# Kernel tuning notes

Measured on AMD Instinct MI355X. Metric: run time of the kernel, lower is better.

The kernel has to match this reference:

```python
import jax, jax.numpy as jnp
import numpy as np

B, S, N, F = 8, 512, 1024, 32   # batch, seq_len, num_nodes, num_features
H = 64                          # hidden_dim
G0 = H // 2                     # first gcn output (32)
K = 3                           # tcn kernel size


def setup_inputs() -> dict:
    key = jax.random.key(0)
    ks = jax.random.split(key, 20)

    def w(k, shape, fan_in):
        return (jax.random.normal(k, shape, dtype=jnp.float32)
                * jnp.asarray(1.0 / np.sqrt(fan_in), jnp.float32))

    return {
        "x":   jax.random.normal(ks[0], (B, S, N, F), dtype=jnp.float32),
        "adj": jax.random.uniform(ks[1], (N, N), dtype=jnp.float32),
        # GCN layer 0: F -> G0 ; layer 1: G0 -> H  (weights stored [in,out])
        "gcn_w0": w(ks[2], (F, G0), F),  "gcn_b0": jnp.zeros((G0,), jnp.float32),
        "gcn_w1": w(ks[3], (G0, H), G0), "gcn_b1": jnp.zeros((H,), jnp.float32),
        # TCN conv weights [out_ch, in_ch, k]
        "conv_w0": w(ks[4], (H, H, K), H * K), "conv_b0": jnp.zeros((H,), jnp.float32),
        "conv_w1": w(ks[5], (H, H, K), H * K), "conv_b1": jnp.zeros((H,), jnp.float32),
        "conv_w2": w(ks[6], (H, H, K), H * K), "conv_b2": jnp.zeros((H,), jnp.float32),
        # fusion Linear(H->H), predictor Linear(H->H//2) -> Linear(H//2->1)
        "fusion_w": w(ks[7], (H, H), H),       "fusion_b": jnp.zeros((H,), jnp.float32),
        "pred_w1": w(ks[8], (H, H // 2), H),   "pred_b1": jnp.zeros((H // 2,), jnp.float32),
        "pred_w2": w(ks[9], (H // 2, 1), H // 2), "pred_b2": jnp.zeros((1,), jnp.float32),
    }


def _normalize_adj(adj):
    # A' = A + I ; D^{-1/2} A' D^{-1/2}   (inf -> 0 guard as in torch code)
    a = adj + jnp.eye(adj.shape[0], dtype=adj.dtype)
    deg = a.sum(axis=1)
    dis = jnp.where(deg > 0, jax.lax.rsqrt(deg), jnp.zeros_like(deg))
    return dis[:, None] * a * dis[None, :]


def _causal_conv(x, w, b, dilation):
    # x: [B, C_in, S], w: [C_out, C_in, K] -> left-pad only == torch pad+trim
    pad = (w.shape[-1] - 1) * dilation
    y = jax.lax.conv_general_dilated(
        x, w, window_strides=(1,), padding=[(pad, 0)],
        rhs_dilation=(dilation,), dimension_numbers=("NCH", "OIH", "NCH"))
    return jax.nn.relu(y + b[None, :, None])  # dropout = identity (eval)


def reference(x, adj, gcn_w0, gcn_b0, gcn_w1, gcn_b1,
              conv_w0, conv_b0, conv_w1, conv_b1, conv_w2, conv_b2,
              fusion_w, fusion_b, pred_w1, pred_b1, pred_w2, pred_b2):
    # adjacency normalization is identical for every timestep/layer: do once
    an = _normalize_adj(adj)  # [N, N]

    # GCN over all timesteps at once (vectorized over the seq loop)
    h = jax.nn.relu(jnp.einsum("mn,bsnf->bsmf", an, x @ gcn_w0) + gcn_b0)
    h = jax.nn.relu(jnp.einsum("mn,bsnf->bsmf", an, h @ gcn_w1) + gcn_b1)

    spatial = h.mean(axis=2)                    # [B, S, H] mean over nodes
    t = jnp.transpose(spatial, (0, 2, 1))       # [B, H, S]

    t = _causal_conv(t, conv_w0, conv_b0, dilation=1)
    t = _causal_conv(t, conv_w1, conv_b1, dilation=2)
    t = _causal_conv(t, conv_w2, conv_b2, dilation=4)

    last = t[:, :, -1]                          # [B, H]
    fused = jax.nn.relu(last @ fusion_w + fusion_b)
    out = jax.nn.relu(fused @ pred_w1 + pred_b1) @ pred_w2 + pred_b2
    return out                                  # [B, 1]
```

## Files before the change

### kernel.cpp

```cpp
#include <hip/hip_runtime.h>
#include <hip/hip_bf16.h>

#define B_   8
#define S_   512
#define N_   1024
#define F_   32
#define H_   64
#define G0_  32
#define T_   15
#define BT_  (B_ * T_)
#define C1_  (BT_ * G0_)

typedef __bf16 bfx8 __attribute__((ext_vector_type(8)));
typedef __bf16 bfx4 __attribute__((ext_vector_type(4)));
typedef float  f32x4 __attribute__((ext_vector_type(4)));

__device__ __forceinline__ void async16(void* l, const void* g) {
    __builtin_amdgcn_global_load_lds(
        (__attribute__((address_space(1))) const void*)g,
        (__attribute__((address_space(3))) void*)l, 16, 0, 0);
}

__global__ void k_deg(const float* __restrict__ adj, float* __restrict__ dis) {
    int r = blockIdx.x;
    int tid = threadIdx.x;
    const float* row = adj + (size_t)r * N_;
    float p = 0.f;
    for (int n = tid; n < N_; n += 256) p += row[n];
    __shared__ float red[256];
    red[tid] = p;
    __syncthreads();
    for (int s = 128; s > 0; s >>= 1) {
        if (tid < s) red[tid] += red[tid + s];
        __syncthreads();
    }
    if (tid == 0) {
        float deg = red[0] + 1.0f;
        dis[r] = (deg > 0.f) ? rsqrtf(deg) : 0.f;
    }
}

__global__ void k_an(const float* __restrict__ adj, const float* __restrict__ dis,
                     __bf16* __restrict__ an) {
    int idx = (blockIdx.x * 256 + threadIdx.x) * 4;
    int m = idx >> 10, n0 = idx & 1023;
    float dm = dis[m];
    float4 a = *(const float4*)&adj[idx];
    float v[4] = {a.x, a.y, a.z, a.w};
    bfx4 o;
#pragma unroll
    for (int j = 0; j < 4; ++j) {
        float vv = v[j] + ((n0 + j) == m ? 1.0f : 0.0f);
        o[j] = (__bf16)(dm * vv * dis[n0 + j]);
    }
    *(bfx4*)&an[idx] = o;
}

__global__ void k_xw0(const float* __restrict__ x, const float* __restrict__ w0,
                      __bf16* __restrict__ xw0t) {
    int bt = blockIdx.y, n0 = blockIdx.x * 32, tid = threadIdx.x;
    int b = bt / T_, tau = bt % T_, s = S_ - T_ + tau;
    __shared__ float xs[32][33];
    __shared__ float w0s[32 * 32];
    const float* xp = x + ((size_t)((b * S_ + s) * N_ + n0)) * F_;
    {
        int r = tid >> 3, c4 = (tid & 7) * 4;
        *(float4*)&xs[r][c4] = *(const float4*)&xp[r * 32 + c4];
        *(float4*)&w0s[tid * 4] = *(const float4*)&w0[tid * 4];
    }
    __syncthreads();
    int g = tid >> 3, nb = (tid & 7) * 4;
    float a0 = 0.f, a1 = 0.f, a2 = 0.f, a3 = 0.f;
#pragma unroll
    for (int f = 0; f < 32; ++f) {
        float wv = w0s[f * 32 + g];
        a0 += xs[nb + 0][f] * wv;
        a1 += xs[nb + 1][f] * wv;
        a2 += xs[nb + 2][f] * wv;
        a3 += xs[nb + 3][f] * wv;
    }
    bfx4 o;
    o[0] = (__bf16)a0; o[1] = (__bf16)a1; o[2] = (__bf16)a2; o[3] = (__bf16)a3;
    *(bfx4*)&xw0t[(size_t)(bt * 32 + g) * N_ + n0 + nb] = o;
}

template <int MODE>
__global__ __launch_bounds__(256) void k_mm(const __bf16* __restrict__ A,
                                            const __bf16* __restrict__ Bm,
                                            void* __restrict__ Cv,
                                            const float* __restrict__ bias) {
    __shared__ __bf16 As[2][128 * 64];
    __shared__ __bf16 Bs[2][128 * 64];
    int tid = threadIdx.x;
    int lane = tid & 63, wv = tid >> 6;
    int rb = blockIdx.y * 128;
    int cb = blockIdx.x * 128;
    int wr = (wv >> 1) * 64, wc = (wv & 1) * 64;

    f32x4 acc[4][4] = {};

    int srow = lane >> 3;
    int scol = ((lane & 7) ^ (srow & 7)) * 8;
    const __bf16* gA = A  + (size_t)(rb + wv * 32 + srow) * 1024 + scol;
    const __bf16* gB = Bm + (size_t)(cb + wv * 32 + srow) * 1024 + scol;

    const int c16 = lane & 15;
    const int qa  = (lane >> 4) * 8;

#pragma unroll
    for (int i = 0; i < 4; ++i) {
        async16(&As[0][(wv * 32 + i * 8) * 64], gA + (size_t)i * 8 * 1024);
        async16(&Bs[0][(wv * 32 + i * 8) * 64], gB + (size_t)i * 8 * 1024);
    }
    __syncthreads();

    int cur = 0;
    for (int t = 0; t < 16; ++t) {
        if (t + 1 < 16) {
            const __bf16* pA = gA + (t + 1) * 64;
            const __bf16* pB = gB + (t + 1) * 64;
#pragma unroll
            for (int i = 0; i < 4; ++i) {
                async16(&As[cur ^ 1][(wv * 32 + i * 8) * 64], pA + (size_t)i * 8 * 1024);
                async16(&Bs[cur ^ 1][(wv * 32 + i * 8) * 64], pB + (size_t)i * 8 * 1024);
            }
        }
#pragma unroll
        for (int kk = 0; kk < 2; ++kk) {
            bfx8 af[4], bfv[4];
#pragma unroll
            for (int r = 0; r < 4; ++r) {
                int row = wr + 16 * r + c16;
                int col = (kk * 64 + qa * 2) ^ ((row & 7) << 4);
                af[r] = *(const bfx8*)((const char*)&As[cur][0] + row * 128 + col);
            }
#pragma unroll
            for (int c = 0; c < 4; ++c) {
                int row = wc + 16 * c + c16;
                int col = (kk * 64 + qa * 2) ^ ((row & 7) << 4);
                bfv[c] = *(const bfx8*)((const char*)&Bs[cur][0] + row * 128 + col);
            }
#pragma unroll
            for (int r = 0; r < 4; ++r)
#pragma unroll
                for (int c = 0; c < 4; ++c)
                    acc[r][c] = __builtin_amdgcn_mfma_f32_16x16x32_bf16(
                        af[r], bfv[c], acc[r][c], 0, 0, 0);
        }
        __syncthreads();
        cur ^= 1;
    }

    int quad = lane >> 4;
    if (MODE == 1) {
        __bf16* C = (__bf16*)Cv;
        float be = bias[c16], bo = bias[c16 + 16];
#pragma unroll
        for (int cj = 0; cj < 4; ++cj) {
            size_t cc = (size_t)(cb + wc + 16 * cj + c16);
            float bg = (cj & 1) ? bo : be;
#pragma unroll
            for (int r = 0; r < 4; ++r) {
                int m4 = rb + wr + 16 * r + quad * 4;
                f32x4 v = acc[r][cj];
                bfx4 o;
#pragma unroll
                for (int j = 0; j < 4; ++j) o[j] = (__bf16)fmaxf(v[j] + bg, 0.f);
                *(bfx4*)&C[cc * 1024 + m4] = o;
            }
        }
    } else {
        float* C = (float*)Cv;
#pragma unroll
        for (int cj = 0; cj < 4; ++cj) {
            size_t cc = (size_t)(cb + wc + 16 * cj + c16);
#pragma unroll
            for (int r = 0; r < 4; ++r) {
                int m4 = rb + wr + 16 * r + quad * 4;
                *(f32x4*)&C[cc * 1024 + m4] = acc[r][cj];
            }
        }
    }
}

__global__ __launch_bounds__(256) void k_h2mean(const float* __restrict__ AGT,
                                                const float* __restrict__ w1,
                                                const float* __restrict__ b1,
                                                float* __restrict__ spatialP) {
    int blk = blockIdx.x;
    int bt = blk >> 2, q = blk & 3;
    int tid = threadIdx.x;
    int h = tid & 63, sub = tid >> 6;
    float w1r[32];
#pragma unroll
    for (int g = 0; g < 32; ++g) w1r[g] = w1[g * 64 + h];
    float bh = b1[h];
    float acc = 0.f;
    const float* base = AGT + (size_t)(bt * 32) * 1024 + q * 256 + sub * 64;
    for (int mq = 0; mq < 16; ++mq) {
        float v0 = bh, v1 = bh, v2 = bh, v3 = bh;
#pragma unroll
        for (int g = 0; g < 32; ++g) {
            float4 a = *(const float4*)(base + (size_t)g * 1024 + mq * 4);
            v0 += a.x * w1r[g];
            v1 += a.y * w1r[g];
            v2 += a.z * w1r[g];
            v3 += a.w * w1r[g];
        }
        acc += fmaxf(v0, 0.f) + fmaxf(v1, 0.f) + fmaxf(v2, 0.f) + fmaxf(v3, 0.f);
    }
    __shared__ float red[4][64];
    red[sub][h] = acc;
    __syncthreads();
    if (tid < 64) {
        spatialP[(size_t)blk * 64 + tid] =
            red[0][tid] + red[1][tid] + red[2][tid] + red[3][tid];
    }
}

__global__ __launch_bounds__(256) void k_head(const float* __restrict__ spatialP,
                       const float* __restrict__ cw0, const float* __restrict__ cb0,
                       const float* __restrict__ cw1, const float* __restrict__ cb1,
                       const float* __restrict__ cw2, const float* __restrict__ cb2,
                       const float* __restrict__ fw,  const float* __restrict__ fb,
                       const float* __restrict__ pw1, const float* __restrict__ pb1,
                       const float* __restrict__ pw2, const float* __restrict__ pb2,
                       float* __restrict__ out) {
    int b = blockIdx.x, tid = threadIdx.x;
    int o = tid & 63, ti = tid >> 6;
    __shared__ float wbuf[3 * 64 * 65];
    __shared__ float sp[15][64], c0s[15][64], c1s[15][64];
    __shared__ float lastv[64], fusedv[64], p1s[32];

    for (int j = tid; j < 15 * 64; j += 256) {
        int t = j >> 6, i = j & 63;
        const float* P = spatialP + ((size_t)(b * 15 + t) * 4) * 64 + i;
        ((float*)sp)[j] = (P[0] + P[64] + P[128] + P[192]) * (1.0f / N_);
    }
    for (int j = tid; j < 12288; j += 256) {
        int oo = j / 192, r = j % 192, ii = r / 3, kk = r % 3;
        wbuf[kk * 4160 + ii * 65 + oo] = cw0[j];
    }
    __syncthreads();
    for (int t4 = ti; t4 < 7; t4 += 4) {
        int t = 2 + 2 * t4;
        float v = cb0[o];
#pragma unroll
        for (int k = 0; k < 3; ++k) {
            const float* in = sp[t - 2 + k];
            const float* wk = &wbuf[k * 4160];
#pragma unroll
            for (int i = 0; i < 64; ++i) v += wk[i * 65 + o] * in[i];
        }
        c0s[t][o] = fmaxf(v, 0.f);
    }
    __syncthreads();
    for (int j = tid; j < 12288; j += 256) {
        int oo = j / 192, r = j % 192, ii = r / 3, kk = r % 3;
        wbuf[kk * 4160 + ii * 65 + oo] = cw1[j];
    }
    __syncthreads();
    if (ti < 3) {
        int t = 6 + 4 * ti;
        float v = cb1[o];
#pragma unroll
        for (int k = 0; k < 3; ++k) {
            const float* in = c0s[t - (2 - k) * 2];
            const float* wk = &wbuf[k * 4160];
#pragma unroll
            for (int i = 0; i < 64; ++i) v += wk[i * 65 + o] * in[i];
        }
        c1s[t][o] = fmaxf(v, 0.f);
    }
    __syncthreads();
    for (int j = tid; j < 12288; j += 256) {
        int oo = j / 192, r = j % 192, ii = r / 3, kk = r % 3;
        wbuf[kk * 4160 + ii * 65 + oo] = cw2[j];
    }
    __syncthreads();
    if (ti == 0) {
        float v = cb2[o];
#pragma unroll
        for (int k = 0; k < 3; ++k) {
            const float* in = c1s[14 - (2 - k) * 4];
            const float* wk = &wbuf[k * 4160];
#pragma unroll
            for (int i = 0; i < 64; ++i) v += wk[i * 65 + o] * in[i];
        }
        lastv[o] = fmaxf(v, 0.f);
    }
    __syncthreads();
    if (ti == 0) {
        float v = fb[o];
#pragma unroll
        for (int i = 0; i < 64; ++i) v += lastv[i] * fw[i * 64 + o];
        fusedv[o] = fmaxf(v, 0.f);
    }
    __syncthreads();
    if (tid < 32) {
        float v = pb1[tid];
#pragma unroll
        for (int i = 0; i < 64; ++i) v += fusedv[i] * pw1[i * 32 + tid];
        p1s[tid] = fmaxf(v, 0.f);
    }
    __syncthreads();
    if (tid == 0) {
        float v = pb2[0];
#pragma unroll
        for (int i = 0; i < 32; ++i) v += p1s[i] * pw2[i];
        out[b] = v;
    }
}

extern "C" void kernel_launch(void* const* d_in, const int* in_sizes, int n_in,
                              void* d_out, int out_size, void* d_ws, size_t ws_size,
                              hipStream_t stream) {
    (void)in_sizes; (void)n_in; (void)out_size; (void)ws_size;
    const float* x   = (const float*)d_in[0];
    const float* adj = (const float*)d_in[1];
    const float* w0  = (const float*)d_in[2];
    const float* b0  = (const float*)d_in[3];
    const float* w1  = (const float*)d_in[4];
    const float* b1  = (const float*)d_in[5];
    const float* cw0 = (const float*)d_in[6];
    const float* cb0 = (const float*)d_in[7];
    const float* cw1 = (const float*)d_in[8];
    const float* cb1 = (const float*)d_in[9];
    const float* cw2 = (const float*)d_in[10];
    const float* cb2 = (const float*)d_in[11];
    const float* fw  = (const float*)d_in[12];
    const float* fb  = (const float*)d_in[13];
    const float* pw1 = (const float*)d_in[14];
    const float* pb1 = (const float*)d_in[15];
    const float* pw2 = (const float*)d_in[16];
    const float* pb2 = (const float*)d_in[17];
    float* outp = (float*)d_out;

    char* w = (char*)d_ws;
    float*  dis      = (float*)(w);
    __bf16* an       = (__bf16*)(w + 4096);
    __bf16* xw0t     = (__bf16*)(w + 4096 + 2097152);
    __bf16* h1t      = (__bf16*)(w + 4096 + 2097152 + 7864320);
    float*  agt      = (float*) (w + 4096 + 2097152 + 2 * 7864320);
    float*  spatialP = (float*) (w + 4096 + 2097152 + 2 * 7864320 + 15728640);

    k_deg<<<N_, 256, 0, stream>>>(adj, dis);
    k_an<<<(N_ * N_) / 1024, 256, 0, stream>>>(adj, dis, an);
    k_xw0<<<dim3(N_ / 32, BT_), 256, 0, stream>>>(x, w0, xw0t);
    k_mm<1><<<dim3(C1_ / 128, N_ / 128), 256, 0, stream>>>(an, xw0t, (void*)h1t, b0);
    k_mm<0><<<dim3(C1_ / 128, N_ / 128), 256, 0, stream>>>(an, h1t, (void*)agt, nullptr);
    k_h2mean<<<BT_ * 4, 256, 0, stream>>>(agt, w1, b1, spatialP);
    k_head<<<B_, 256, 0, stream>>>(spatialP, cw0, cb0, cw1, cb1, cw2, cb2,
                                   fw, fb, pw1, pb1, pw2, pb2, outp);
}
```

Baseline: 712.5 us.

## Use eight-wave GEMM blocks and pre-transpose TCN conv weights in a prep kernel

```diff
diff --git a/kernel.cpp b/kernel.cpp
--- a/kernel.cpp
+++ b/kernel.cpp
@@ -54,6 +54,16 @@
         o[j] = (__bf16)(dm * vv * dis[n0 + j]);
     }
     *(bfx4*)&an[idx] = o;
+}
+
+__global__ void k_wprep(const float* __restrict__ cw0, const float* __restrict__ cw1,
+                        const float* __restrict__ cw2, float* __restrict__ wp) {
+    int idx = blockIdx.x * 256 + threadIdx.x;
+    if (idx >= 3 * 12480) return;
+    int layer = idx / 12480, r = idx % 12480;
+    int kk = r / 4160, r2 = r % 4160, ii = r2 / 65, oo = r2 % 65;
+    const float* src = (layer == 0) ? cw0 : ((layer == 1) ? cw1 : cw2);
+    wp[idx] = (oo < 64) ? src[oo * 192 + ii * 3 + kk] : 0.f;
 }
 
 __global__ void k_xw0(const float* __restrict__ x, const float* __restrict__ w0,
@@ -85,7 +95,7 @@
 }
 
 template <int MODE>
-__global__ __launch_bounds__(256) void k_mm(const __bf16* __restrict__ A,
+__global__ __launch_bounds__(512) void k_mm(const __bf16* __restrict__ A,
                                             const __bf16* __restrict__ Bm,
                                             void* __restrict__ Cv,
                                             const float* __restrict__ bias) {
@@ -95,22 +105,23 @@
     int lane = tid & 63, wv = tid >> 6;
     int rb = blockIdx.y * 128;
     int cb = blockIdx.x * 128;
-    int wr = (wv >> 1) * 64, wc = (wv & 1) * 64;
-
-    f32x4 acc[4][4] = {};
+    int wr = (wv >> 2) * 64;
+    int wc = (wv & 3) * 32;
+
+    f32x4 acc[4][2] = {};
 
     int srow = lane >> 3;
     int scol = ((lane & 7) ^ (srow & 7)) * 8;
-    const __bf16* gA = A  + (size_t)(rb + wv * 32 + srow) * 1024 + scol;
-    const __bf16* gB = Bm + (size_t)(cb + wv * 32 + srow) * 1024 + scol;
+    const __bf16* gA = A  + (size_t)(rb + wv * 16 + srow) * 1024 + scol;
+    const __bf16* gB = Bm + (size_t)(cb + wv * 16 + srow) * 1024 + scol;
 
     const int c16 = lane & 15;
     const int qa  = (lane >> 4) * 8;
 
 #pragma unroll
-    for (int i = 0; i < 4; ++i) {
-        async16(&As[0][(wv * 32 + i * 8) * 64], gA + (size_t)i * 8 * 1024);
-        async16(&Bs[0][(wv * 32 + i * 8) * 64], gB + (size_t)i * 8 * 1024);
+    for (int i = 0; i < 2; ++i) {
+        async16(&As[0][(wv * 16 + i * 8) * 64], gA + (size_t)i * 8 * 1024);
+        async16(&Bs[0][(wv * 16 + i * 8) * 64], gB + (size_t)i * 8 * 1024);
     }
     __syncthreads();
 
@@ -120,14 +131,14 @@
             const __bf16* pA = gA + (t + 1) * 64;
             const __bf16* pB = gB + (t + 1) * 64;
 #pragma unroll
-            for (int i = 0; i < 4; ++i) {
-                async16(&As[cur ^ 1][(wv * 32 + i * 8) * 64], pA + (size_t)i * 8 * 1024);
-                async16(&Bs[cur ^ 1][(wv * 32 + i * 8) * 64], pB + (size_t)i * 8 * 1024);
+            for (int i = 0; i < 2; ++i) {
+                async16(&As[cur ^ 1][(wv * 16 + i * 8) * 64], pA + (size_t)i * 8 * 1024);
+                async16(&Bs[cur ^ 1][(wv * 16 + i * 8) * 64], pB + (size_t)i * 8 * 1024);
             }
         }
 #pragma unroll
         for (int kk = 0; kk < 2; ++kk) {
-            bfx8 af[4], bfv[4];
+            bfx8 af[4], bfv[2];
 #pragma unroll
             for (int r = 0; r < 4; ++r) {
                 int row = wr + 16 * r + c16;
@@ -135,7 +146,7 @@
                 af[r] = *(const bfx8*)((const char*)&As[cur][0] + row * 128 + col);
             }
 #pragma unroll
-            for (int c = 0; c < 4; ++c) {
+            for (int c = 0; c < 2; ++c) {
                 int row = wc + 16 * c + c16;
                 int col = (kk * 64 + qa * 2) ^ ((row & 7) << 4);
                 bfv[c] = *(const bfx8*)((const char*)&Bs[cur][0] + row * 128 + col);
@@ -143,7 +154,7 @@
 #pragma unroll
             for (int r = 0; r < 4; ++r)
 #pragma unroll
-                for (int c = 0; c < 4; ++c)
+                for (int c = 0; c < 2; ++c)
                     acc[r][c] = __builtin_amdgcn_mfma_f32_16x16x32_bf16(
                         af[r], bfv[c], acc[r][c], 0, 0, 0);
         }
@@ -156,7 +167,7 @@
         __bf16* C = (__bf16*)Cv;
         float be = bias[c16], bo = bias[c16 + 16];
 #pragma unroll
-        for (int cj = 0; cj < 4; ++cj) {
+        for (int cj = 0; cj < 2; ++cj) {
             size_t cc = (size_t)(cb + wc + 16 * cj + c16);
             float bg = (cj & 1) ? bo : be;
 #pragma unroll
@@ -172,7 +183,7 @@
     } else {
         float* C = (float*)Cv;
 #pragma unroll
-        for (int cj = 0; cj < 4; ++cj) {
+        for (int cj = 0; cj < 2; ++cj) {
             size_t cc = (size_t)(cb + wc + 16 * cj + c16);
 #pragma unroll
             for (int r = 0; r < 4; ++r) {
@@ -219,9 +230,9 @@
 }
 
 __global__ __launch_bounds__(256) void k_head(const float* __restrict__ spatialP,
-                       const float* __restrict__ cw0, const float* __restrict__ cb0,
-                       const float* __restrict__ cw1, const float* __restrict__ cb1,
-                       const float* __restrict__ cw2, const float* __restrict__ cb2,
+                       const float* __restrict__ wp,
+                       const float* __restrict__ cb0, const float* __restrict__ cb1,
+                       const float* __restrict__ cb2,
                        const float* __restrict__ fw,  const float* __restrict__ fb,
                        const float* __restrict__ pw1, const float* __restrict__ pb1,
                        const float* __restrict__ pw2, const float* __restrict__ pb2,
@@ -237,10 +248,8 @@
         const float* P = spatialP + ((size_t)(b * 15 + t) * 4) * 64 + i;
         ((float*)sp)[j] = (P[0] + P[64] + P[128] + P[192]) * (1.0f / N_);
     }
-    for (int j = tid; j < 12288; j += 256) {
-        int oo = j / 192, r = j % 192, ii = r / 3, kk = r % 3;
-        wbuf[kk * 4160 + ii * 65 + oo] = cw0[j];
-    }
+    for (int j4 = tid; j4 < 3120; j4 += 256)
+        *(float4*)&wbuf[j4 * 4] = *(const float4*)&wp[j4 * 4];
     __syncthreads();
     for (int t4 = ti; t4 < 7; t4 += 4) {
         int t = 2 + 2 * t4;
@@ -255,10 +264,8 @@
         c0s[t][o] = fmaxf(v, 0.f);
     }
     __syncthreads();
-    for (int j = tid; j < 12288; j += 256) {
-        int oo = j / 192, r = j % 192, ii = r / 3, kk = r % 3;
-        wbuf[kk * 4160 + ii * 65 + oo] = cw1[j];
-    }
+    for (int j4 = tid; j4 < 3120; j4 += 256)
+        *(float4*)&wbuf[j4 * 4] = *(const float4*)&wp[12480 + j4 * 4];
     __syncthreads();
     if (ti < 3) {
         int t = 6 + 4 * ti;
@@ -273,10 +280,8 @@
         c1s[t][o] = fmaxf(v, 0.f);
     }
     __syncthreads();
-    for (int j = tid; j < 12288; j += 256) {
-        int oo = j / 192, r = j % 192, ii = r / 3, kk = r % 3;
-        wbuf[kk * 4160 + ii * 65 + oo] = cw2[j];
-    }
+    for (int j4 = tid; j4 < 3120; j4 += 256)
+        *(float4*)&wbuf[j4 * 4] = *(const float4*)&wp[24960 + j4 * 4];
     __syncthreads();
     if (ti == 0) {
         float v = cb2[o];
@@ -343,13 +348,15 @@
     __bf16* h1t      = (__bf16*)(w + 4096 + 2097152 + 7864320);
     float*  agt      = (float*) (w + 4096 + 2097152 + 2 * 7864320);
     float*  spatialP = (float*) (w + 4096 + 2097152 + 2 * 7864320 + 15728640);
+    float*  wp       = (float*) (w + 4096 + 2097152 + 2 * 7864320 + 15728640 + 122880);
 
     k_deg<<<N_, 256, 0, stream>>>(adj, dis);
     k_an<<<(N_ * N_) / 1024, 256, 0, stream>>>(adj, dis, an);
+    k_wprep<<<147, 256, 0, stream>>>(cw0, cw1, cw2, wp);
     k_xw0<<<dim3(N_ / 32, BT_), 256, 0, stream>>>(x, w0, xw0t);
-    k_mm<1><<<dim3(C1_ / 128, N_ / 128), 256, 0, stream>>>(an, xw0t, (void*)h1t, b0);
-    k_mm<0><<<dim3(C1_ / 128, N_ / 128), 256, 0, stream>>>(an, h1t, (void*)agt, nullptr);
+    k_mm<1><<<dim3(C1_ / 128, N_ / 128), 512, 0, stream>>>(an, xw0t, (void*)h1t, b0);
+    k_mm<0><<<dim3(C1_ / 128, N_ / 128), 512, 0, stream>>>(an, h1t, (void*)agt, nullptr);
     k_h2mean<<<BT_ * 4, 256, 0, stream>>>(agt, w1, b1, spatialP);
-    k_head<<<B_, 256, 0, stream>>>(spatialP, cw0, cb0, cw1, cb1, cw2, cb2,
+    k_head<<<B_, 256, 0, stream>>>(spatialP, wp, cb0, cb1, cb2,
                                    fw, fb, pw1, pb1, pw2, pb2, outp);
 }
```

Measured after the change: 699.7 us. About the same (-1.8%).
